# Kernel optimization log

Hardware: AMD Instinct MI355X
Metric: run time of the kernel (lower is better)

Reference implementation:

```python
import jax, jax.numpy as jnp
import numpy as np

jax.config.update("jax_enable_x64", True)  # original upcasts to double for cdist

B, D, T = 16, 256, 2048
K = 1024  # num_embeddings
COMMITMENT_COST = 0.25


def setup_inputs() -> dict:
    key = jax.random.key(0)
    k1, k2 = jax.random.split(key)
    inputs = jax.random.normal(k1, (B, D, T), dtype=jnp.float32)
    embeddings = jax.random.uniform(k2, (K, D), minval=-1.0 / K, maxval=1.0 / K, dtype=jnp.float32)
    return {"inputs": inputs, "embeddings": embeddings}


def reference(inputs, embeddings):
    b, d, t = inputs.shape
    # [B, D, T] -> [B*T, D]
    flat = jnp.transpose(inputs, (0, 2, 1)).reshape(-1, d)
    # fp64 pairwise squared distances (argmin identical to cdist p=2)
    x = flat.astype(jnp.float64)
    e = embeddings.astype(jnp.float64)
    d2 = (jnp.sum(x * x, axis=1, keepdims=True)
          - 2.0 * (x @ e.T)
          + jnp.sum(e * e, axis=1))  # [N, K]
    encoding_indices = jnp.argmin(d2, axis=1)  # [N]
    quantized = embeddings[encoding_indices].reshape(b, t, d).transpose(0, 2, 1)  # [B, D, T]
    q_detached = jax.lax.stop_gradient(quantized)
    e_latent_loss = jnp.mean((q_detached - inputs) ** 2)
    q_latent_loss = jnp.mean((quantized - jax.lax.stop_gradient(inputs)) ** 2)
    loss = q_latent_loss + COMMITMENT_COST * e_latent_loss
    # straight-through estimator
    quantized_st = inputs + jax.lax.stop_gradient(quantized - inputs)
    return quantized_st, loss, e_latent_loss, q_latent_loss, encoding_indices
```

## Files before the change

kernel.cpp:

```cpp
#include <hip/hip_runtime.h>
#include <hip/hip_bf16.h>

#define NB 16
#define ND 256
#define NT 2048
#define NK 1024
#define NN (NB * NT)
#define QSIZE (NB * ND * NT)
#define SCL_OFF QSIZE
#define IDX_OFF (QSIZE + 3)
#define TAU 4.0e-5f
#define NSLICE 4

#define WS_E2F   0
#define WS_E2D   4096
#define WS_CNT   12288
#define WS_PART  12352
#define WS_LIST  20544
#define WS_B1S   86080
#define WS_I1S   610368
#define WS_M12   872512
#define WS_BPACK 1134656

typedef __attribute__((ext_vector_type(8))) short bf16x8;
typedef __attribute__((ext_vector_type(4))) float f32x4;
#define MFMA16(a, b, c) __builtin_amdgcn_mfma_f32_16x16x32_bf16(a, b, c, 0, 0, 0)

__device__ inline void bf16split(float v, short& hi, short& lo) {
    union { __hip_bfloat16 b; short s; } uh, ul;
    uh.b = __float2bfloat16(v);
    float hf = __bfloat162float(uh.b);
    ul.b = __float2bfloat16(v - hf);
    hi = uh.s; lo = ul.s;
}

__global__ __launch_bounds__(64) void vq_prep(const float4* __restrict__ E4,
                                              double* __restrict__ e2d,
                                              float* __restrict__ e2f,
                                              uint4* __restrict__ Bp4,
                                              int* __restrict__ cnt) {
    const int k = blockIdx.x;
    const int lane = threadIdx.x;
    float4 v = E4[k * 64 + lane];
    float4 a, b2v;
    a.x = __shfl(v.x, 2 * lane, 64); a.y = __shfl(v.y, 2 * lane, 64);
    a.z = __shfl(v.z, 2 * lane, 64); a.w = __shfl(v.w, 2 * lane, 64);
    b2v.x = __shfl(v.x, 2 * lane + 1, 64); b2v.y = __shfl(v.y, 2 * lane + 1, 64);
    b2v.z = __shfl(v.z, 2 * lane + 1, 64); b2v.w = __shfl(v.w, 2 * lane + 1, 64);
    if (lane < 32) {
        const int ds = lane >> 2, q = lane & 3;
        const int cc = k >> 4;
        const int fl = q * 16 + (k & 15);
        float vals[8] = {a.x, a.y, a.z, a.w, b2v.x, b2v.y, b2v.z, b2v.w};
        union { short s[8]; uint4 u; } hi, lo;
        #pragma unroll
        for (int j = 0; j < 8; ++j) bf16split(vals[j], hi.s[j], lo.s[j]);
        Bp4[(size_t)cc * 1024 + ds * 64 + fl]       = hi.u;
        Bp4[(size_t)cc * 1024 + 512 + ds * 64 + fl] = lo.u;
    }
    double s = (double)v.x * v.x + (double)v.y * v.y + (double)v.z * v.z + (double)v.w * v.w;
    #pragma unroll
    for (int off = 32; off; off >>= 1) s += __shfl_down(s, off, 64);
    if (lane == 0) { e2d[k] = s; e2f[k] = (float)s; }
    if (k == 0 && lane == 0) cnt[0] = 0;
}

__global__ __launch_bounds__(256, 2) void vq_pass1(const float* __restrict__ X,
                                                   const uint4* __restrict__ Bp4,
                                                   const float* __restrict__ e2f,
                                                   float* __restrict__ b1s,
                                                   unsigned short* __restrict__ i1s,
                                                   unsigned short* __restrict__ m12s) {
    __shared__ uint4 Bl4[2][1024];
    const int tid   = threadIdx.x;
    const int lane  = tid & 63;
    const int w     = tid >> 6;
    const int slice = blockIdx.x & 3;
    const int n0    = (blockIdx.x >> 2) * 128;
    const int b     = n0 >> 11;
    const int t0    = n0 & (NT - 1);
    const int m16   = lane & 15;
    const int q     = lane >> 4;
    const uint4* Bps = Bp4 + (size_t)slice * 16384;

    bf16x8 ah[2][8], al[2][8];
    const float* Xb = X + (size_t)b * (ND * NT);
    #pragma unroll
    for (int t = 0; t < 2; ++t) {
        const int trow = t0 + w * 32 + t * 16 + m16;
        #pragma unroll
        for (int ds = 0; ds < 8; ++ds) {
            #pragma unroll
            for (int j = 0; j < 8; ++j) {
                const int d = ds * 32 + q * 8 + j;
                float v = Xb[(size_t)d * NT + trow];
                short h, l; bf16split(v, h, l);
                ah[t][ds][j] = h; al[t][ds][j] = l;
            }
        }
    }

    float b1[2][4], b2[2][4]; int i1[2][4];
    #pragma unroll
    for (int t = 0; t < 2; ++t)
        #pragma unroll
        for (int r = 0; r < 4; ++r) { b1[t][r] = 3e38f; b2[t][r] = 3e38f; i1[t][r] = 0; }

    uint4 pre[4];
    #pragma unroll
    for (int i = 0; i < 4; ++i) pre[i] = Bps[tid + 256 * i];
    #pragma unroll
    for (int i = 0; i < 4; ++i) Bl4[0][tid + 256 * i] = pre[i];
    __syncthreads();

    for (int cc = 0; cc < 16; ++cc) {
        const bf16x8* Bf = (const bf16x8*)Bl4[cc & 1];
        if (cc < 15) {
            #pragma unroll
            for (int i = 0; i < 4; ++i) pre[i] = Bps[(size_t)(cc + 1) * 1024 + tid + 256 * i];
        }
        f32x4 hh0 = {0.f,0.f,0.f,0.f}, lh0 = {0.f,0.f,0.f,0.f}, hl0 = {0.f,0.f,0.f,0.f};
        f32x4 hh1 = {0.f,0.f,0.f,0.f}, lh1 = {0.f,0.f,0.f,0.f}, hl1 = {0.f,0.f,0.f,0.f};
        #pragma unroll
        for (int ds = 0; ds < 8; ++ds) {
            bf16x8 bh = Bf[ds * 64 + lane];
            bf16x8 bl = Bf[512 + ds * 64 + lane];
            hh0 = MFMA16(ah[0][ds], bh, hh0);
            hh1 = MFMA16(ah[1][ds], bh, hh1);
            lh0 = MFMA16(al[0][ds], bh, lh0);
            lh1 = MFMA16(al[1][ds], bh, lh1);
            hl0 = MFMA16(ah[0][ds], bl, hl0);
            hl1 = MFMA16(ah[1][ds], bl, hl1);
        }
        if (cc < 15) {
            #pragma unroll
            for (int i = 0; i < 4; ++i) Bl4[(cc + 1) & 1][tid + 256 * i] = pre[i];
            __syncthreads();
        }
        const int  code = slice * 256 + cc * 16 + m16;
        const float e2v = e2f[code];
        #pragma unroll
        for (int r = 0; r < 4; ++r) {
            float s0 = e2v - 2.0f * (hh0[r] + lh0[r] + hl0[r]);
            if (s0 < b1[0][r]) { b2[0][r] = b1[0][r]; b1[0][r] = s0; i1[0][r] = code; }
            else if (s0 < b2[0][r]) b2[0][r] = s0;
            float s1 = e2v - 2.0f * (hh1[r] + lh1[r] + hl1[r]);
            if (s1 < b1[1][r]) { b2[1][r] = b1[1][r]; b1[1][r] = s1; i1[1][r] = code; }
            else if (s1 < b2[1][r]) b2[1][r] = s1;
        }
    }

    #pragma unroll
    for (int t = 0; t < 2; ++t) {
        #pragma unroll
        for (int r = 0; r < 4; ++r) {
            float B1 = b1[t][r], B2 = b2[t][r]; int I1 = i1[t][r];
            #pragma unroll
            for (int mm = 1; mm < 16; mm <<= 1) {
                float o1 = __shfl_xor(B1, mm, 16);
                float o2 = __shfl_xor(B2, mm, 16);
                int   oi = __shfl_xor(I1, mm, 16);
                if (o1 < B1 || (o1 == B1 && oi < I1)) { B2 = fminf(B1, o2); B1 = o1; I1 = oi; }
                else B2 = fminf(B2, o1);
            }
            if (m16 == 0) {
                int n = n0 + w * 32 + t * 16 + q * 4 + r;
                size_t s = (size_t)slice * NN + n;
                b1s[s] = B1;
                i1s[s] = (unsigned short)I1;
                m12s[s] = (unsigned short)fminf(65535.0f, rintf((B2 - B1) * 1.0e8f));
            }
        }
    }
}

__global__ __launch_bounds__(256) void vq_merge(const float4* __restrict__ E4,
                                                const float* __restrict__ b1s,
                                                const unsigned short* __restrict__ i1s,
                                                const unsigned short* __restrict__ m12s,
                                                int* __restrict__ cnt,
                                                unsigned short* __restrict__ list,
                                                float* __restrict__ ET,
                                                float* __restrict__ out) {
    const int tid = threadIdx.x;
    const int gid = blockIdx.x * 256 + tid;
    {
        const int k = gid >> 5;
        const int p = gid & 31;
        float4 v0 = E4[(size_t)k * 64 + p * 2];
        float4 v1 = E4[(size_t)k * 64 + p * 2 + 1];
        const int d0 = p * 8;
        ET[(size_t)(d0 + 0) * NK + k] = v0.x; ET[(size_t)(d0 + 1) * NK + k] = v0.y;
        ET[(size_t)(d0 + 2) * NK + k] = v0.z; ET[(size_t)(d0 + 3) * NK + k] = v0.w;
        ET[(size_t)(d0 + 4) * NK + k] = v1.x; ET[(size_t)(d0 + 5) * NK + k] = v1.y;
        ET[(size_t)(d0 + 6) * NK + k] = v1.z; ET[(size_t)(d0 + 7) * NK + k] = v1.w;
    }
    const int n = gid;
    float B1 = b1s[n]; int I1 = i1s[n];
    float B2 = B1 + (float)m12s[n] * 1.0e-8f;
    #pragma unroll
    for (int s = 1; s < NSLICE; ++s) {
        float c1 = b1s[(size_t)s * NN + n];
        float c2 = c1 + (float)m12s[(size_t)s * NN + n] * 1.0e-8f;
        int   ci = i1s[(size_t)s * NN + n];
        if (c1 < B1) { B2 = fminf(B1, c2); B1 = c1; I1 = ci; }
        else          B2 = fminf(B2, c1);
    }
    out[IDX_OFF + n] = (float)I1;
    const bool flag = (B2 - B1 < TAU);
    unsigned long long mask = __ballot(flag);
    int wcnt = __popcll(mask);
    int base = 0;
    if ((tid & 63) == 0 && wcnt) base = atomicAdd(cnt, wcnt);
    base = __shfl(base, 0, 64);
    if (flag) {
        int pos = base + __popcll(mask & ((1ull << (tid & 63)) - 1ull));
        list[pos] = (unsigned short)n;
    }
}

__global__ __launch_bounds__(256, 2) void vq_refine(const float* __restrict__ X,
                                                    const float4* __restrict__ ET4,
                                                    const double* __restrict__ e2d,
                                                    const int* __restrict__ cnt,
                                                    const unsigned short* __restrict__ list,
                                                    float* __restrict__ out) {
    __shared__ double xs[2][256];
    __shared__ double sm_s[4][2];
    __shared__ int    sm_k[4][2];
    __shared__ int    sm_n[2];
    const int m = cnt[0];
    const int tid = threadIdx.x;
    for (int j0 = blockIdx.x * 2; j0 < m; j0 += 2048) {
        if (tid < 2) {
            int j = j0 + tid;
            sm_n[tid] = (int)list[j < m ? j : m - 1];
        }
        __syncthreads();
        #pragma unroll
        for (int g = 0; g < 2; ++g) {
            int n = sm_n[g]; int bb = n >> 11; int tt = n & (NT - 1);
            xs[g][tid] = (double)X[((size_t)bb * ND + tid) * NT + tt];
        }
        __syncthreads();
        double acc[4][2];
        #pragma unroll
        for (int kk = 0; kk < 4; ++kk) { acc[kk][0] = 0.0; acc[kk][1] = 0.0; }
        #pragma unroll 4
        for (int dd = 0; dd < 256; ++dd) {
            float4 ev = ET4[(size_t)dd * 256 + tid];
            double x0 = xs[0][dd], x1 = xs[1][dd];
            acc[0][0] += x0 * (double)ev.x; acc[0][1] += x1 * (double)ev.x;
            acc[1][0] += x0 * (double)ev.y; acc[1][1] += x1 * (double)ev.y;
            acc[2][0] += x0 * (double)ev.z; acc[2][1] += x1 * (double)ev.z;
            acc[3][0] += x0 * (double)ev.w; acc[3][1] += x1 * (double)ev.w;
        }
        #pragma unroll
        for (int g = 0; g < 2; ++g) {
            double bs = 1e300; int bk = 0x7fffffff;
            #pragma unroll
            for (int kk = 0; kk < 4; ++kk) {
                int k = 4 * tid + kk;
                double s = e2d[k] - 2.0 * acc[kk][g];
                if (s < bs) { bs = s; bk = k; }
            }
            #pragma unroll
            for (int mm = 1; mm < 64; mm <<= 1) {
                double os = __shfl_xor(bs, mm, 64);
                int    ok = __shfl_xor(bk, mm, 64);
                if (os < bs || (os == bs && ok < bk)) { bs = os; bk = ok; }
            }
            if ((tid & 63) == 0) { sm_s[tid >> 6][g] = bs; sm_k[tid >> 6][g] = bk; }
        }
        __syncthreads();
        if (tid < 2 && j0 + tid < m) {
            double Bv = 1e300; int Kv = 0x7fffffff;
            #pragma unroll
            for (int ww = 0; ww < 4; ++ww) {
                double s2 = sm_s[ww][tid]; int k2 = sm_k[ww][tid];
                if (s2 < Bv || (s2 == Bv && k2 < Kv)) { Bv = s2; Kv = k2; }
            }
            out[IDX_OFF + sm_n[tid]] = (float)Kv;
        }
        __syncthreads();
    }
}

__global__ __launch_bounds__(256) void vq_gather(const float* __restrict__ X,
                                                 const float4* __restrict__ E4,
                                                 float* __restrict__ out,
                                                 double* __restrict__ part) {
    __shared__ float Eq[32 * 257];
    __shared__ double sm[4];
    const int bt = blockIdx.x;
    const int b  = bt >> 6;
    const int t0 = (bt & 63) << 5;
    const float* irowf = out + IDX_OFF + b * NT + t0;
    {
        const int r  = threadIdx.x >> 3;
        const int l8 = threadIdx.x & 7;
        const int id = (int)irowf[r];
        const float4* er = E4 + (size_t)id * 64;
        #pragma unroll
        for (int it = 0; it < 8; ++it) {
            int c = l8 + (it << 3);
            float4 v = er[c];
            float* p = &Eq[r * 257 + 4 * c];
            p[0] = v.x; p[1] = v.y; p[2] = v.z; p[3] = v.w;
        }
    }
    __syncthreads();
    const int tw = threadIdx.x & 31;
    const int dg = threadIdx.x >> 5;
    double ls = 0.0;
    #pragma unroll 8
    for (int it = 0; it < 32; ++it) {
        const int d = dg + (it << 3);
        const float qv = Eq[tw * 257 + d];
        const size_t off = ((size_t)b * ND + d) * NT + t0 + tw;
        const float x = X[off];
        out[off] = x + (qv - x);
        const double df = (double)qv - (double)x;
        ls = fma(df, df, ls);
    }
    #pragma unroll
    for (int o = 32; o; o >>= 1) ls += __shfl_down(ls, o, 64);
    if ((threadIdx.x & 63) == 0) sm[threadIdx.x >> 6] = ls;
    __syncthreads();
    if (threadIdx.x == 0) part[bt] = sm[0] + sm[1] + sm[2] + sm[3];
}

__global__ __launch_bounds__(256) void vq_final(const double* __restrict__ part,
                                                float* __restrict__ out) {
    __shared__ double sm[4];
    const int tid = threadIdx.x;
    double s = part[tid] + part[tid + 256] + part[tid + 512] + part[tid + 768];
    #pragma unroll
    for (int o = 32; o; o >>= 1) s += __shfl_down(s, o, 64);
    if ((tid & 63) == 0) sm[tid >> 6] = s;
    __syncthreads();
    if (tid == 0) {
        double mse = (sm[0] + sm[1] + sm[2] + sm[3]) * (1.0 / (double)QSIZE);
        out[SCL_OFF + 0] = (float)(1.25 * mse);
        out[SCL_OFF + 1] = (float)mse;
        out[SCL_OFF + 2] = (float)mse;
    }
}

extern "C" void kernel_launch(void* const* d_in, const int* in_sizes, int n_in,
                              void* d_out, int out_size, void* d_ws, size_t ws_size,
                              hipStream_t stream) {
    const float* X = (const float*)d_in[0];
    const float* E = (const float*)d_in[1];
    float* out = (float*)d_out;

    char* ws = (char*)d_ws;
    float*  e2f   = (float*) (ws + WS_E2F);
    double* e2d   = (double*)(ws + WS_E2D);
    int*    cnt   = (int*)   (ws + WS_CNT);
    double* part  = (double*)(ws + WS_PART);
    unsigned short* list = (unsigned short*)(ws + WS_LIST);
    float*  b1s   = (float*) (ws + WS_B1S);
    unsigned short* i1s  = (unsigned short*)(ws + WS_I1S);
    unsigned short* m12s = (unsigned short*)(ws + WS_M12);
    uint4*  bpack = (uint4*) (ws + WS_BPACK);
    float*  et    = (float*) (ws + WS_BPACK);

    vq_prep  <<<NK, 64, 0, stream>>>((const float4*)E, e2d, e2f, bpack, cnt);
    vq_pass1 <<<(NN / 128) * NSLICE, 256, 0, stream>>>(X, bpack, e2f, b1s, i1s, m12s);
    vq_merge <<<NN / 256, 256, 0, stream>>>((const float4*)E, b1s, i1s, m12s, cnt, list, et, out);
    vq_refine<<<1024, 256, 0, stream>>>(X, (const float4*)et, e2d, cnt, list, out);
    vq_gather<<<NB * (NT / 32), 256, 0, stream>>>(X, (const float4*)E, out, part);
    vq_final <<<1, 256, 0, stream>>>(part, out);
}
```

Measured before the change: 201.0 us.

## Pre-pack inputs into bf16 hi/lo MFMA fragment layout in a separate kernel

Adds a vq_prep_x kernel that reads X with coalesced float4 loads, splits each value into bf16 hi/lo, transposes through LDS and writes fragment-ordered packed data into the output buffer as scratch. Pass1 then loads its A fragments with two uint4 loads per slice instead of 64 strided scalar loads plus conversions. This removes the uncoalesced strided reads of X, which each pass1 slice repeated four times. In exchange it adds a kernel launch and a full extra write and read of a packed copy of X. It also relies on later kernels overwriting the output buffer before it is read.

Result: slower. 217.9 us (+8.4%).

```diff
diff --git a/kernel.cpp b/kernel.cpp
--- a/kernel.cpp
+++ b/kernel.cpp
@@ -65,7 +65,39 @@
     if (k == 0 && lane == 0) cnt[0] = 0;
 }
 
-__global__ __launch_bounds__(256, 2) void vq_pass1(const float* __restrict__ X,
+__global__ __launch_bounds__(256) void vq_prep_x(const float4* __restrict__ X4,
+                                                 uint4* __restrict__ Xp4) {
+    __shared__ unsigned int L[8 * 536];
+    const int tile = blockIdx.x;
+    const int tid  = threadIdx.x;
+    const int b    = tile >> 7;
+    const int t0   = (tile & 127) * 16;
+    const float4* src = X4 + (((size_t)(b * ND + tid) * NT + t0) >> 2);
+    float4 f0 = src[0], f1 = src[1], f2 = src[2], f3 = src[3];
+    float vals[16] = {f0.x,f0.y,f0.z,f0.w, f1.x,f1.y,f1.z,f1.w,
+                      f2.x,f2.y,f2.z,f2.w, f3.x,f3.y,f3.z,f3.w};
+    const int ds = tid >> 5, q = (tid >> 3) & 3, j = tid & 7;
+    const int base = ds * 536 + q * 132 + j;
+    #pragma unroll
+    for (int m = 0; m < 16; ++m) {
+        short h, l; bf16split(vals[m], h, l);
+        L[base + m * 8] = (unsigned int)(unsigned short)h |
+                          ((unsigned int)(unsigned short)l << 16);
+    }
+    __syncthreads();
+    uint4* outp = Xp4 + (size_t)tile * 1024;
+    #pragma unroll
+    for (int k4 = 0; k4 < 4; ++k4) {
+        const int widx = tid * 16 + k4 * 4;
+        const int dsw  = widx >> 9;
+        const int lane_o = (widx & 511) >> 3;
+        const int j0   = widx & 7;
+        const int qw = lane_o >> 4, m16 = lane_o & 15;
+        outp[tid * 4 + k4] = *(const uint4*)&L[dsw * 536 + qw * 132 + m16 * 8 + j0];
+    }
+}
+
+__global__ __launch_bounds__(256, 2) void vq_pass1(const uint4* __restrict__ Xp4,
                                                    const uint4* __restrict__ Bp4,
                                                    const float* __restrict__ e2f,
                                                    float* __restrict__ b1s,
@@ -77,26 +109,29 @@
     const int w     = tid >> 6;
     const int slice = blockIdx.x & 3;
     const int n0    = (blockIdx.x >> 2) * 128;
-    const int b     = n0 >> 11;
-    const int t0    = n0 & (NT - 1);
     const int m16   = lane & 15;
     const int q     = lane >> 4;
     const uint4* Bps = Bp4 + (size_t)slice * 16384;
 
     bf16x8 ah[2][8], al[2][8];
-    const float* Xb = X + (size_t)b * (ND * NT);
+    const int tileb = (n0 >> 4) + w * 2;
     #pragma unroll
     for (int t = 0; t < 2; ++t) {
-        const int trow = t0 + w * 32 + t * 16 + m16;
         #pragma unroll
         for (int ds = 0; ds < 8; ++ds) {
-            #pragma unroll
-            for (int j = 0; j < 8; ++j) {
-                const int d = ds * 32 + q * 8 + j;
-                float v = Xb[(size_t)d * NT + trow];
-                short h, l; bf16split(v, h, l);
-                ah[t][ds][j] = h; al[t][ds][j] = l;
-            }
+            const size_t base = ((size_t)(tileb + t) * 8 + ds) * 128 + lane * 2;
+            uint4 w0 = Xp4[base];
+            uint4 w1 = Xp4[base + 1];
+            union { unsigned int u[4]; bf16x8 v; } H, Lo;
+            H.u[0]  = (w0.x & 0xffffu) | (w0.y << 16);
+            H.u[1]  = (w0.z & 0xffffu) | (w0.w << 16);
+            H.u[2]  = (w1.x & 0xffffu) | (w1.y << 16);
+            H.u[3]  = (w1.z & 0xffffu) | (w1.w << 16);
+            Lo.u[0] = (w0.x >> 16) | (w0.y & 0xffff0000u);
+            Lo.u[1] = (w0.z >> 16) | (w0.w & 0xffff0000u);
+            Lo.u[2] = (w1.x >> 16) | (w1.y & 0xffff0000u);
+            Lo.u[3] = (w1.z >> 16) | (w1.w & 0xffff0000u);
+            ah[t][ds] = H.v; al[t][ds] = Lo.v;
         }
     }
 
@@ -365,9 +400,12 @@
     unsigned short* m12s = (unsigned short*)(ws + WS_M12);
     uint4*  bpack = (uint4*) (ws + WS_BPACK);
     float*  et    = (float*) (ws + WS_BPACK);
+    uint4*  xpack = (uint4*) out;
 
     vq_prep  <<<NK, 64, 0, stream>>>((const float4*)E, e2d, e2f, bpack, cnt);
-    vq_pass1 <<<(NN / 128) * NSLICE, 256, 0, stream>>>(X, bpack, e2f, b1s, i1s, m12s);
+    vq_prep_x<<<NN / 16, 256, 0, stream>>>((const float4*)X, xpack);
+    vq_pass1 <<<(NN / 128) * NSLICE, 256, 0, stream>>>((const uint4*)xpack, bpack, e2f,
+                                                       b1s, i1s, m12s);
     vq_merge <<<NN / 256, 256, 0, stream>>>((const float4*)E, b1s, i1s, m12s, cnt, list, et, out);
     vq_refine<<<1024, 256, 0, stream>>>(X, (const float4*)et, e2d, cnt, list, out);
     vq_gather<<<NB * (NT / 32), 256, 0, stream>>>(X, (const float4*)E, out, part);
```
